# Optimization experiments

Measured on AMD Instinct MI355X. Metric: run time of the kernel, lower is better.

Reference implementation:

```python
import jax, jax.numpy as jnp
import numpy as np

B, L, C, H = 16, 680, 1024, 16
PATCH_NUMS = [1, 4, 9, 16, 25, 36, 64, 100, 169, 256]  # per-scale token counts, sum == L
MAX_SCALE_LOG = float(np.log(100.0))


def setup_inputs() -> dict:
    key = jax.random.key(0)
    ks = jax.random.split(key, 4)
    return {
        "x": jax.random.normal(ks[0], (B, L, C), jnp.float32),
        "patch_nums": jnp.asarray(PATCH_NUMS, jnp.int32),
        "mat_qkv_w": (jax.random.normal(ks[1], (3 * C, C), jnp.float32) * 0.02),
        "q_bias": jnp.zeros((C,), jnp.float32),
        "v_bias": jnp.zeros((C,), jnp.float32),
        "scale_log": jnp.full((1, H, 1, 1), np.log(4.0), jnp.float32),
        "proj_w": (jax.random.normal(ks[2], (C, C), jnp.float32) * 0.02),
        "proj_b": jnp.zeros((C,), jnp.float32),
    }


def _l2norm(t):
    # F.normalize(dim=-1): x / max(||x||_2, eps)
    n = jnp.sqrt(jnp.sum(t * t, axis=-1, keepdims=True))
    return t / jnp.maximum(n, 1e-12)


def reference(x, patch_nums, mat_qkv_w, q_bias, v_bias, scale_log, proj_w, proj_b):
    b, l, c = x.shape
    h = scale_log.shape[1]
    d = c // h
    # fused QKV linear with bias = cat(q_bias, zeros, v_bias)
    bias = jnp.concatenate([q_bias, jnp.zeros_like(q_bias), v_bias])
    qkv = (x @ mat_qkv_w.T + bias).reshape(b, l, 3, h, d)
    q, k, v = qkv[:, :, 0], qkv[:, :, 1], qkv[:, :, 2]  # [B, L, H, D]
    # attn_l2_norm path: scale=1, learned per-head multiplier on normalized q
    scale_mul = jnp.exp(jnp.minimum(scale_log, MAX_SCALE_LOG)).transpose(0, 2, 1, 3)  # (1,1,H,1)
    q = _l2norm(q) * scale_mul
    k = _l2norm(k)
    # training path: block-diagonal varlen attention, one block per scale
    pn = np.asarray(patch_nums).tolist()  # static scale schedule
    outs, start = [], 0
    for ln in pn:
        qs = q[:, start:start + ln]
        ks_ = k[:, start:start + ln]
        vs = v[:, start:start + ln]
        s = jnp.einsum("bihd,bjhd->bhij", qs, ks_)  # softmax_scale = 1
        a = jax.nn.softmax(s, axis=-1)
        outs.append(jnp.einsum("bhij,bjhd->bihd", a, vs))
        start += ln
    oup = jnp.concatenate(outs, axis=1).reshape(b, l, c)
    return oup @ proj_w.T + proj_b
```

## Files before the change

### kernel.cpp

```cpp
#include <hip/hip_runtime.h>

typedef __attribute__((ext_vector_type(8))) short bf16x8;
typedef __attribute__((ext_vector_type(4))) float f32x4;

#define Hh   16
#define Ll   680
#define Cc   1024
#define Bb   16
#define NSEG 10
#define LPAD 720

__device__ __forceinline__ unsigned short f32_bf16(float f) {
  union { float f; unsigned int u; } x; x.f = f;
  unsigned int r = x.u + 0x7FFFu + ((x.u >> 16) & 1u);
  return (unsigned short)(r >> 16);
}
__device__ __forceinline__ float bf16_f32(unsigned short u) {
  union { unsigned int u; float f; } x; x.u = ((unsigned int)u) << 16;
  return x.f;
}

__device__ __forceinline__ void async_copy16(const unsigned short* g, unsigned short* l) {
  __builtin_amdgcn_global_load_lds(
      (const __attribute__((address_space(1))) unsigned int*)g,
      (__attribute__((address_space(3))) unsigned int*)l, 16, 0, 0);
}

__device__ __constant__ int c_start2[11] = {0,1,5,14,30,55,91,155,255,424,680};
__device__ __constant__ int c_ps[NSEG]   = {0,8,16,32,48,80,120,184,288,464};
__device__ __constant__ int c_seg[16]    = {0,1,2,3,4,5,6,7,7,8,8,8,9,9,9,9};
__device__ __constant__ int c_tile0[16]  = {0,0,0,0,0,0,0,0,4,0,4,8,0,4,8,12};
__device__ __constant__ int c_len[NSEG]  = {1,4,9,16,25,36,64,100,169,256};

struct PlTab { unsigned short v[Ll]; };
constexpr PlTab make_pl() {
  PlTab t{};
  int starts[11] = {0,1,5,14,30,55,91,155,255,424,680};
  int ps[10]     = {0,8,16,32,48,80,120,184,288,464};
  for (int s = 0; s < 10; ++s)
    for (int l = starts[s]; l < starts[s + 1]; ++l)
      t.v[l] = (unsigned short)(l - starts[s] + ps[s]);
  return t;
}
__device__ __constant__ PlTab c_plt = make_pl();

__global__ __launch_bounds__(256) void conv_all(const float* __restrict__ x,
                                                const float* __restrict__ wqkv,
                                                const float* __restrict__ wproj,
                                                unsigned short* __restrict__ xb,
                                                unsigned short* __restrict__ wqkvb,
                                                unsigned short* __restrict__ wprojb) {
  const size_t n1 = (size_t)Bb * Ll * Cc;
  const size_t n2 = n1 + (size_t)3 * Cc * Cc;
  const size_t n3 = n2 + (size_t)Cc * Cc;
  size_t i = ((size_t)blockIdx.x * 256 + threadIdx.x) * 4;
  if (i >= n3) return;
  const float* src; unsigned short* dst; size_t off;
  if (i < n1)      { src = x;     dst = xb;     off = i; }
  else if (i < n2) { src = wqkv;  dst = wqkvb;  off = i - n1; }
  else             { src = wproj; dst = wprojb; off = i - n2; }
  float4 v = *reinterpret_cast<const float4*>(src + off);
  ushort4 o;
  o.x = f32_bf16(v.x); o.y = f32_bf16(v.y); o.z = f32_bf16(v.z); o.w = f32_bf16(v.w);
  *reinterpret_cast<ushort4*>(dst + off) = o;
}

__global__ __launch_bounds__(512, 2) void gemm_qkv(const unsigned short* __restrict__ A,
                                                   const unsigned short* __restrict__ Bm,
                                                   const float* __restrict__ qb,
                                                   const float* __restrict__ vb,
                                                   unsigned short* __restrict__ qn,
                                                   unsigned short* __restrict__ kn,
                                                   unsigned short* __restrict__ vtb) {
  __shared__ __align__(16) unsigned short lds[73728];
  const int t = threadIdx.x;
  const int lane = t & 63, w = t >> 6;
  const int col = lane & 15, quad = lane >> 4;
  const int wn = (w >> 1) * 64;
  const int m0 = blockIdx.y * 128, n0 = blockIdx.x * 256;
  const int bhs = wn >> 7;

  auto stageA = [&](int d3, int hs, int k0) {
    int kc = k0 > 960 ? 960 : k0;
    int r = t >> 3;
    int part = (t & 7) ^ (r & 7);
    async_copy16(A + (size_t)(m0 + hs * 64 + r) * 1024 + kc + part * 8,
                 lds + (d3 * 2 + hs) * 4096 + w * 512);
  };
  auto stageB = [&](int d3, int hs, int k0) {
    int kc = k0 > 960 ? 960 : k0;
#pragma unroll
    for (int i = 0; i < 2; ++i) {
      int c = i * 512 + t;
      int r = c >> 3;
      int part = (c & 7) ^ (r & 7);
      async_copy16(Bm + (size_t)(n0 + hs * 128 + r) * 1024 + kc + part * 8,
                   lds + 24576 + (d3 * 2 + hs) * 8192 + (i * 512 + w * 64) * 8);
    }
  };

  f32x4 acc[4][4];
#pragma unroll
  for (int i = 0; i < 4; ++i)
#pragma unroll
    for (int j = 0; j < 4; ++j)
#pragma unroll
      for (int r = 0; r < 4; ++r) acc[i][j][r] = 0.f;

#pragma unroll
  for (int tt = 0; tt < 2; ++tt) {
    stageB(tt, 0, tt * 64); stageA(tt, 0, tt * 64);
    stageB(tt, 1, tt * 64); stageA(tt, 1, tt * 64);
  }
  stageB(2, 0, 128); stageA(2, 0, 128);
  asm volatile("s_waitcnt vmcnt(9)" ::: "memory");
  __builtin_amdgcn_s_barrier();
  __builtin_amdgcn_sched_barrier(0);

  int bsel = 0;
  for (int tt = 0; tt < 16; ++tt) {
    const int b  = bsel;
    const int b2 = (bsel + 2 >= 3) ? bsel - 1 : bsel + 2;
    const unsigned short* As0 = lds + (b * 2 + 0) * 4096;
    const unsigned short* As1 = lds + (b * 2 + 1) * 4096;
    const unsigned short* Bs  = lds + 24576 + (b * 2 + bhs) * 8192;
    bf16x8 bfr[4][2], af[2][2];

#pragma unroll
    for (int nf = 0; nf < 4; ++nf) {
      int rb = (wn & 64) + nf * 16 + col;
#pragma unroll
      for (int kq = 0; kq < 2; ++kq)
        bfr[nf][kq] = *reinterpret_cast<const bf16x8*>(
            &Bs[(rb * 8 + ((kq * 4 + quad) ^ (col & 7))) * 8]);
    }
#pragma unroll
    for (int j = 0; j < 2; ++j) {
      int ri = (w & 1) * 32 + j * 16 + col;
#pragma unroll
      for (int kq = 0; kq < 2; ++kq)
        af[j][kq] = *reinterpret_cast<const bf16x8*>(
            &As0[(ri * 8 + ((kq * 4 + quad) ^ (col & 7))) * 8]);
    }
    stageB(b2, 1, (tt + 2) * 64);
    stageA(b2, 1, (tt + 2) * 64);
    __builtin_amdgcn_s_barrier();
    __builtin_amdgcn_s_setprio(1);
#pragma unroll
    for (int j = 0; j < 2; ++j)
#pragma unroll
      for (int nf = 0; nf < 4; ++nf)
#pragma unroll
        for (int kq = 0; kq < 2; ++kq)
          acc[j][nf] = __builtin_amdgcn_mfma_f32_16x16x32_bf16(af[j][kq], bfr[nf][kq],
                                                               acc[j][nf], 0, 0, 0);
    __builtin_amdgcn_s_setprio(0);
    __builtin_amdgcn_sched_barrier(0);
    asm volatile("s_waitcnt vmcnt(6)" ::: "memory");
    __builtin_amdgcn_s_barrier();
    __builtin_amdgcn_sched_barrier(0);

#pragma unroll
    for (int j = 0; j < 2; ++j) {
      int ri = (w & 1) * 32 + j * 16 + col;
#pragma unroll
      for (int kq = 0; kq < 2; ++kq)
        af[j][kq] = *reinterpret_cast<const bf16x8*>(
            &As1[(ri * 8 + ((kq * 4 + quad) ^ (col & 7))) * 8]);
    }
    stageB(b, 0, (tt + 3) * 64);
    stageA(b, 0, (tt + 3) * 64);
    __builtin_amdgcn_s_barrier();
    __builtin_amdgcn_s_setprio(1);
#pragma unroll
    for (int j = 0; j < 2; ++j)
#pragma unroll
      for (int nf = 0; nf < 4; ++nf)
#pragma unroll
        for (int kq = 0; kq < 2; ++kq)
          acc[2 + j][nf] = __builtin_amdgcn_mfma_f32_16x16x32_bf16(af[j][kq], bfr[nf][kq],
                                                                   acc[2 + j][nf], 0, 0, 0);
    __builtin_amdgcn_s_setprio(0);
    __builtin_amdgcn_sched_barrier(0);
    asm volatile("s_waitcnt vmcnt(9)" ::: "memory");
    __builtin_amdgcn_s_barrier();
    __builtin_amdgcn_sched_barrier(0);

    bsel = (bsel == 2) ? 0 : bsel + 1;
  }

  const int nbase = n0 + wn;
  const int field = nbase >> 10;
  const int h = (nbase >> 6) & 15;

  if (field < 2) {
    float scl[4][4];
    if (field == 1) {
#pragma unroll
      for (int mi = 0; mi < 4; ++mi)
#pragma unroll
        for (int r = 0; r < 4; ++r) {
          float s = 0.f;
#pragma unroll
          for (int ni = 0; ni < 4; ++ni) s += acc[mi][ni][r] * acc[mi][ni][r];
          s += __shfl_xor(s, 1); s += __shfl_xor(s, 2);
          s += __shfl_xor(s, 4); s += __shfl_xor(s, 8);
          scl[mi][r] = 1.f / fmaxf(sqrtf(s), 1e-12f);
        }
    }
    unsigned short* dst0 = (field == 0) ? qn : kn;
#pragma unroll
    for (int ni = 0; ni < 4; ++ni) {
      const int d = ni * 16 + col;
      const float bv = (field == 0) ? qb[h * 64 + d] : 0.f;
#pragma unroll
      for (int mi = 0; mi < 4; ++mi)
#pragma unroll
        for (int r = 0; r < 4; ++r) {
          int gm = m0 + (mi >> 1) * 64 + (w & 1) * 32 + (mi & 1) * 16 + quad * 4 + r;
          int b = gm / 680, l = gm - b * 680;
          float v = (field == 0) ? (acc[mi][ni][r] + bv) : (acc[mi][ni][r] * scl[mi][r]);
          dst0[((size_t)(b * Hh + h) * Ll + l) * 64 + d] = f32_bf16(v);
        }
    }
  } else {
#pragma unroll
    for (int mi = 0; mi < 4; ++mi) {
      int pl4[4], bb4[4];
#pragma unroll
      for (int r = 0; r < 4; ++r) {
        int gm = m0 + (mi >> 1) * 64 + (w & 1) * 32 + (mi & 1) * 16 + quad * 4 + r;
        int b = gm / 680, l = gm - b * 680;
        pl4[r] = c_plt.v[l];
        bb4[r] = b;
      }
#pragma unroll
      for (int ni = 0; ni < 4; ++ni) {
        const int d = ni * 16 + col;
        const float bv = vb[h * 64 + d];
#pragma unroll
        for (int r = 0; r < 4; ++r)
          vtb[((size_t)(bb4[r] * Hh + h) * 64 + d) * LPAD + pl4[r]] =
              f32_bf16(acc[mi][ni][r] + bv);
      }
    }
  }
}

__global__ __launch_bounds__(256) void gemm_bt(const unsigned short* __restrict__ A,
                                               const unsigned short* __restrict__ Bm,
                                               const float* __restrict__ bias,
                                               float* __restrict__ outp,
                                               int M, int N, int K) {
  __shared__ __align__(16) unsigned short As[128 * 64];
  __shared__ __align__(16) unsigned short Bs[128 * 64];
  const int t = threadIdx.x;
  const int lane = t & 63, w = t >> 6;
  const int col = lane & 15, quad = lane >> 4;
  const int wm = (w & 1) * 64, wn = (w >> 1) * 64;
  const int m0 = blockIdx.y * 128, n0 = blockIdx.x * 128;

  f32x4 acc[4][4];
#pragma unroll
  for (int i = 0; i < 4; ++i)
#pragma unroll
    for (int j = 0; j < 4; ++j)
#pragma unroll
      for (int r = 0; r < 4; ++r) acc[i][j][r] = 0.f;

  const int cbase = w * 256 + lane;
  for (int k0 = 0; k0 < K; k0 += 64) {
    __syncthreads();
#pragma unroll
    for (int i = 0; i < 4; ++i) {
      int c = cbase + i * 64;
      int r = c >> 3;
      int part = (c & 7) ^ (r & 7);
      async_copy16(A + (size_t)(m0 + r) * K + k0 + part * 8, As + (w * 256 + i * 64) * 8);
      async_copy16(Bm + (size_t)(n0 + r) * K + k0 + part * 8, Bs + (w * 256 + i * 64) * 8);
    }
    __syncthreads();
#pragma unroll
    for (int kk = 0; kk < 64; kk += 32) {
      const int p = (kk >> 3) + quad;
      bf16x8 af[4], bfr[4];
#pragma unroll
      for (int mi = 0; mi < 4; ++mi) {
        int row = wm + mi * 16 + col;
        af[mi] = *reinterpret_cast<const bf16x8*>(&As[(row * 8 + (p ^ (col & 7))) * 8]);
      }
#pragma unroll
      for (int ni = 0; ni < 4; ++ni) {
        int row = wn + ni * 16 + col;
        bfr[ni] = *reinterpret_cast<const bf16x8*>(&Bs[(row * 8 + (p ^ (col & 7))) * 8]);
      }
#pragma unroll
      for (int mi = 0; mi < 4; ++mi)
#pragma unroll
        for (int ni = 0; ni < 4; ++ni)
          acc[mi][ni] = __builtin_amdgcn_mfma_f32_16x16x32_bf16(af[mi], bfr[ni], acc[mi][ni], 0, 0, 0);
    }
  }
#pragma unroll
  for (int mi = 0; mi < 4; ++mi)
#pragma unroll
    for (int ni = 0; ni < 4; ++ni) {
      int gn = n0 + wn + ni * 16 + col;
      float bv = bias[gn];
#pragma unroll
      for (int r = 0; r < 4; ++r) {
        int gm = m0 + wm + mi * 16 + quad * 4 + r;
        outp[(size_t)gm * N + gn] = acc[mi][ni][r] + bv;
      }
    }
}

__global__ __launch_bounds__(256) void attn_kernel(const unsigned short* __restrict__ qn,
                                                   const unsigned short* __restrict__ kn,
                                                   const unsigned short* __restrict__ vtb,
                                                   const float* __restrict__ slog,
                                                   unsigned short* __restrict__ outb) {
  __shared__ __align__(16) unsigned short Ks[128 * 64];
  __shared__ __align__(16) unsigned short Vs[64 * 128];
  __shared__ __align__(16) unsigned short Ps[4 * 16 * 132];

  const int t = threadIdx.x;
  const int lane = t & 63, w = t >> 6;
  const int col = lane & 15, quad = lane >> 4;
  const int wi = blockIdx.x >> 8, bh = blockIdx.x & 255;
  const int h = bh & 15;
  const int seg = c_seg[wi];
  const int start = c_start2[seg], ln = c_len[seg], ps = c_ps[seg];
  const int njt = (ln + 15) >> 4;
  const int nchunk = (njt + 7) >> 3;
  const int qt = c_tile0[wi] + w;
  const bool qvalid = qt < njt;
  const float smul = __expf(fminf(slog[h], 4.6051701859880914f));

  const int qi = qt * 16 + col;
  const unsigned short* qrow = qn + ((size_t)bh * Ll + start + qi) * 64;
  bf16x8 qf0 = *reinterpret_cast<const bf16x8*>(qrow + quad * 8);
  bf16x8 qf1 = *reinterpret_cast<const bf16x8*>(qrow + 32 + quad * 8);
  {
    float ss = 0.f;
#pragma unroll
    for (int e = 0; e < 8; ++e) {
      float f0 = bf16_f32((unsigned short)qf0[e]), f1 = bf16_f32((unsigned short)qf1[e]);
      ss += f0 * f0 + f1 * f1;
    }
    ss += __shfl_xor(ss, 16);
    ss += __shfl_xor(ss, 32);
    const float qsc = smul / fmaxf(sqrtf(ss), 1e-12f);
#pragma unroll
    for (int e = 0; e < 8; ++e) {
      qf0[e] = (short)f32_bf16(bf16_f32((unsigned short)qf0[e]) * qsc);
      qf1[e] = (short)f32_bf16(bf16_f32((unsigned short)qf1[e]) * qsc);
    }
  }

  f32x4 o[4];
#pragma unroll
  for (int nt = 0; nt < 4; ++nt)
#pragma unroll
    for (int r = 0; r < 4; ++r) o[nt][r] = 0.f;
  float m4[4] = {-1e30f, -1e30f, -1e30f, -1e30f};
  float l4[4] = {0.f, 0.f, 0.f, 0.f};

  const int jc_t = (t & 15) ^ (t >> 4);

  for (int ch = 0; ch < nchunk; ++ch) {
    const int jbase = ch * 128;
    const int jtc = (njt - ch * 8 > 8) ? 8 : (njt - ch * 8);
    const int jtcp = (jtc + 1) & ~1;
    const int rowsK = jtc * 16;
    const int jcmax = jtcp * 2;
    __syncthreads();

#pragma unroll
    for (int i = 0; i < 4; ++i) {
      int c = i * 256 + w * 64 + lane;
      int jr = c >> 3;
      if (jr < rowsK) {
        int cc = (c & 7) ^ (jr & 7);
        async_copy16(kn + ((size_t)bh * Ll + start + jbase + jr) * 64 + cc * 8,
                     Ks + (i * 256 + w * 64) * 8);
      }
    }
    if (jc_t < jcmax) {
#pragma unroll
      for (int i = 0; i < 4; ++i) {
        int d = i * 16 + (t >> 4);
        async_copy16(vtb + ((size_t)bh * 64 + d) * LPAD + ps + jbase + jc_t * 8,
                     Vs + (i * 256 + w * 64) * 8);
      }
    }
    __syncthreads();

    f32x4 sf[8];
#pragma unroll
    for (int jt = 0; jt < 8; ++jt) {
      if (jt >= jtcp) continue;
      f32x4 s;
#pragma unroll
      for (int r = 0; r < 4; ++r) s[r] = 0.f;
      if (jt < jtc) {
        int jrow = jt * 16 + col;
        bf16x8 k0 = *reinterpret_cast<const bf16x8*>(&Ks[(jrow * 8 + (quad ^ (jrow & 7))) * 8]);
        bf16x8 k1 = *reinterpret_cast<const bf16x8*>(&Ks[(jrow * 8 + ((4 + quad) ^ (jrow & 7))) * 8]);
        s = __builtin_amdgcn_mfma_f32_16x16x32_bf16(qf0, k0, s, 0, 0, 0);
        s = __builtin_amdgcn_mfma_f32_16x16x32_bf16(qf1, k1, s, 0, 0, 0);
      }
      if (jbase + jt * 16 + col >= ln) {
#pragma unroll
        for (int r = 0; r < 4; ++r) s[r] = -1e30f;
      }
      sf[jt] = s;
    }
    float mc[4];
#pragma unroll
    for (int r = 0; r < 4; ++r) mc[r] = sf[0][r];
#pragma unroll
    for (int jt = 1; jt < 8; ++jt) {
      if (jt >= jtcp) continue;
#pragma unroll
      for (int r = 0; r < 4; ++r) mc[r] = fmaxf(mc[r], sf[jt][r]);
    }
#pragma unroll
    for (int mask = 1; mask <= 8; mask <<= 1)
#pragma unroll
      for (int r = 0; r < 4; ++r) mc[r] = fmaxf(mc[r], __shfl_xor(mc[r], mask));
    float alpha[4];
#pragma unroll
    for (int r = 0; r < 4; ++r) {
      float mn = fmaxf(m4[r], mc[r]);
      alpha[r] = __expf(m4[r] - mn);
      m4[r] = mn;
    }
    float ls[4] = {0.f, 0.f, 0.f, 0.f};
#pragma unroll
    for (int jt = 0; jt < 8; ++jt) {
      if (jt >= jtcp) continue;
#pragma unroll
      for (int r = 0; r < 4; ++r) {
        float pv = __expf(sf[jt][r] - m4[r]);
        ls[r] += pv;
        Ps[(w * 16 + quad * 4 + r) * 132 + jt * 16 + col] = f32_bf16(pv);
      }
    }
#pragma unroll
    for (int mask = 1; mask <= 8; mask <<= 1)
#pragma unroll
      for (int r = 0; r < 4; ++r) ls[r] += __shfl_xor(ls[r], mask);
#pragma unroll
    for (int r = 0; r < 4; ++r) l4[r] = l4[r] * alpha[r] + ls[r];
#pragma unroll
    for (int nt = 0; nt < 4; ++nt)
#pragma unroll
      for (int r = 0; r < 4; ++r) o[nt][r] *= alpha[r];

#pragma unroll
    for (int kk2 = 0; kk2 < 4; ++kk2) {
      if (kk2 >= (jtcp >> 1)) continue;
      bf16x8 pf = *reinterpret_cast<const bf16x8*>(&Ps[(w * 16 + col) * 132 + kk2 * 32 + quad * 8]);
#pragma unroll
      for (int nt = 0; nt < 4; ++nt) {
        int d = nt * 16 + col;
        int slot = (kk2 * 4 + quad) ^ (d & 15);
        bf16x8 vf = *reinterpret_cast<const bf16x8*>(&Vs[(d * 16 + slot) * 8]);
        o[nt] = __builtin_amdgcn_mfma_f32_16x16x32_bf16(pf, vf, o[nt], 0, 0, 0);
      }
    }
  }

  if (qvalid) {
    float inv[4];
#pragma unroll
    for (int r = 0; r < 4; ++r) inv[r] = 1.f / l4[r];
    const int b = bh >> 4;
#pragma unroll
    for (int nt = 0; nt < 4; ++nt)
#pragma unroll
      for (int r = 0; r < 4; ++r) {
        int ri = qt * 16 + quad * 4 + r;
        if (ri < ln) {
          size_t off = ((size_t)b * Ll + start + ri) * Cc + h * 64 + nt * 16 + col;
          outb[off] = f32_bf16(o[nt][r] * inv[r]);
        }
      }
  }
}

extern "C" void kernel_launch(void* const* d_in, const int* in_sizes, int n_in,
                              void* d_out, int out_size, void* d_ws, size_t ws_size,
                              hipStream_t stream) {
  const float* x     = (const float*)d_in[0];
  const float* wqkv  = (const float*)d_in[2];
  const float* qbias = (const float*)d_in[3];
  const float* vbias = (const float*)d_in[4];
  const float* slog  = (const float*)d_in[5];
  const float* wproj = (const float*)d_in[6];
  const float* pbias = (const float*)d_in[7];
  float* out = (float*)d_out;

  const size_t nX  = (size_t)Bb * Ll * Cc;
  const size_t nWq = (size_t)3 * Cc * Cc;
  const size_t nWp = (size_t)Cc * Cc;
  const size_t nVt = (size_t)Bb * Hh * 64 * LPAD;

  char* p = (char*)d_ws;
  unsigned short* xb     = (unsigned short*)p;  p += nX * 2;
  unsigned short* wqkvb  = (unsigned short*)p;  p += nWq * 2;
  unsigned short* wprojb = (unsigned short*)p;  p += nWp * 2;
  unsigned short* qn     = (unsigned short*)p;  p += nX * 2;
  unsigned short* kn     = (unsigned short*)p;  p += nX * 2;
  unsigned short* vtb    = (unsigned short*)p;  p += nVt * 2;
  unsigned short* attn   = xb;

  const size_t nAll = nX + nWq + nWp;
  conv_all<<<(int)(nAll / 1024), 256, 0, stream>>>(x, wqkv, wproj, xb, wqkvb, wprojb);

  gemm_qkv<<<dim3(12, 85), 512, 0, stream>>>(xb, wqkvb, qbias, vbias, qn, kn, vtb);
  attn_kernel<<<Bb * Hh * 16, 256, 0, stream>>>(qn, kn, vtb, slog, attn);
  gemm_bt<<<dim3(8, 85), 256, 0, stream>>>(attn, wprojb, pbias, out, 10880, 1024, 1024);
}
```

Before: 318.2 us.

## Rewrite projection GEMM with 128x256 tiles and triple-buffered async pipeline

The output projection GEMM moves from a single-buffered 128x128 tile with 256 threads to a 128x256 tile with 512 threads. K-slices are staged through a three-deep LDS ring using async global-to-LDS copies, with explicit vmcnt waits and barriers so loads overlap MFMA work, plus setprio around the MFMA bursts. This mirrors the pipelined QKV GEMM and targets load-latency stalls between the two syncthreads in the old loop. In exchange it uses about 144 KB of LDS per block and hardcodes the shapes, and the K-offset clamp at 960 issues redundant prefetch loads at the tail.

```diff
diff --git a/kernel.cpp b/kernel.cpp
--- a/kernel.cpp
+++ b/kernel.cpp
@@ -247,72 +247,139 @@
   }
 }
 
-__global__ __launch_bounds__(256) void gemm_bt(const unsigned short* __restrict__ A,
-                                               const unsigned short* __restrict__ Bm,
-                                               const float* __restrict__ bias,
-                                               float* __restrict__ outp,
-                                               int M, int N, int K) {
-  __shared__ __align__(16) unsigned short As[128 * 64];
-  __shared__ __align__(16) unsigned short Bs[128 * 64];
+__global__ __launch_bounds__(512, 2) void gemm_bt(const unsigned short* __restrict__ A,
+                                                  const unsigned short* __restrict__ Bm,
+                                                  const float* __restrict__ bias,
+                                                  float* __restrict__ outp) {
+  __shared__ __align__(16) unsigned short lds[73728];
   const int t = threadIdx.x;
   const int lane = t & 63, w = t >> 6;
   const int col = lane & 15, quad = lane >> 4;
-  const int wm = (w & 1) * 64, wn = (w >> 1) * 64;
-  const int m0 = blockIdx.y * 128, n0 = blockIdx.x * 128;
-
-  f32x4 acc[4][4];
-#pragma unroll
-  for (int i = 0; i < 4; ++i)
-#pragma unroll
-    for (int j = 0; j < 4; ++j)
-#pragma unroll
-      for (int r = 0; r < 4; ++r) acc[i][j][r] = 0.f;
-
-  const int cbase = w * 256 + lane;
-  for (int k0 = 0; k0 < K; k0 += 64) {
-    __syncthreads();
-#pragma unroll
-    for (int i = 0; i < 4; ++i) {
-      int c = cbase + i * 64;
+  const int wn = (w >> 1) * 64;
+  const int m0 = blockIdx.y * 128, n0 = blockIdx.x * 256;
+  const int bhs = wn >> 7;
+
+  auto stageA = [&](int d3, int hs, int k0) {
+    int kc = k0 > 960 ? 960 : k0;
+    int r = t >> 3;
+    int part = (t & 7) ^ (r & 7);
+    async_copy16(A + (size_t)(m0 + hs * 64 + r) * 1024 + kc + part * 8,
+                 lds + (d3 * 2 + hs) * 4096 + w * 512);
+  };
+  auto stageB = [&](int d3, int hs, int k0) {
+    int kc = k0 > 960 ? 960 : k0;
+#pragma unroll
+    for (int i = 0; i < 2; ++i) {
+      int c = i * 512 + t;
       int r = c >> 3;
       int part = (c & 7) ^ (r & 7);
-      async_copy16(A + (size_t)(m0 + r) * K + k0 + part * 8, As + (w * 256 + i * 64) * 8);
-      async_copy16(Bm + (size_t)(n0 + r) * K + k0 + part * 8, Bs + (w * 256 + i * 64) * 8);
-    }
-    __syncthreads();
-#pragma unroll
-    for (int kk = 0; kk < 64; kk += 32) {
-      const int p = (kk >> 3) + quad;
-      bf16x8 af[4], bfr[4];
-#pragma unroll
-      for (int mi = 0; mi < 4; ++mi) {
-        int row = wm + mi * 16 + col;
-        af[mi] = *reinterpret_cast<const bf16x8*>(&As[(row * 8 + (p ^ (col & 7))) * 8]);
-      }
-#pragma unroll
-      for (int ni = 0; ni < 4; ++ni) {
-        int row = wn + ni * 16 + col;
-        bfr[ni] = *reinterpret_cast<const bf16x8*>(&Bs[(row * 8 + (p ^ (col & 7))) * 8]);
-      }
-#pragma unroll
-      for (int mi = 0; mi < 4; ++mi)
-#pragma unroll
-        for (int ni = 0; ni < 4; ++ni)
-          acc[mi][ni] = __builtin_amdgcn_mfma_f32_16x16x32_bf16(af[mi], bfr[ni], acc[mi][ni], 0, 0, 0);
-    }
-  }
-#pragma unroll
-  for (int mi = 0; mi < 4; ++mi)
-#pragma unroll
-    for (int ni = 0; ni < 4; ++ni) {
-      int gn = n0 + wn + ni * 16 + col;
-      float bv = bias[gn];
+      async_copy16(Bm + (size_t)(n0 + hs * 128 + r) * 1024 + kc + part * 8,
+                   lds + 24576 + (d3 * 2 + hs) * 8192 + (i * 512 + w * 64) * 8);
+    }
+  };
+
+  f32x4 acc[4][4];
+#pragma unroll
+  for (int i = 0; i < 4; ++i)
+#pragma unroll
+    for (int j = 0; j < 4; ++j)
+#pragma unroll
+      for (int r = 0; r < 4; ++r) acc[i][j][r] = 0.f;
+
+#pragma unroll
+  for (int tt = 0; tt < 2; ++tt) {
+    stageB(tt, 0, tt * 64); stageA(tt, 0, tt * 64);
+    stageB(tt, 1, tt * 64); stageA(tt, 1, tt * 64);
+  }
+  stageB(2, 0, 128); stageA(2, 0, 128);
+  asm volatile("s_waitcnt vmcnt(9)" ::: "memory");
+  __builtin_amdgcn_s_barrier();
+  __builtin_amdgcn_sched_barrier(0);
+
+  int bsel = 0;
+  for (int tt = 0; tt < 16; ++tt) {
+    const int b  = bsel;
+    const int b2 = (bsel + 2 >= 3) ? bsel - 1 : bsel + 2;
+    const unsigned short* As0 = lds + (b * 2 + 0) * 4096;
+    const unsigned short* As1 = lds + (b * 2 + 1) * 4096;
+    const unsigned short* Bs  = lds + 24576 + (b * 2 + bhs) * 8192;
+    bf16x8 bfr[4][2], af[2][2];
+
+#pragma unroll
+    for (int nf = 0; nf < 4; ++nf) {
+      int rb = (wn & 64) + nf * 16 + col;
+#pragma unroll
+      for (int kq = 0; kq < 2; ++kq)
+        bfr[nf][kq] = *reinterpret_cast<const bf16x8*>(
+            &Bs[(rb * 8 + ((kq * 4 + quad) ^ (col & 7))) * 8]);
+    }
+#pragma unroll
+    for (int j = 0; j < 2; ++j) {
+      int ri = (w & 1) * 32 + j * 16 + col;
+#pragma unroll
+      for (int kq = 0; kq < 2; ++kq)
+        af[j][kq] = *reinterpret_cast<const bf16x8*>(
+            &As0[(ri * 8 + ((kq * 4 + quad) ^ (col & 7))) * 8]);
+    }
+    stageB(b2, 1, (tt + 2) * 64);
+    stageA(b2, 1, (tt + 2) * 64);
+    __builtin_amdgcn_s_barrier();
+    __builtin_amdgcn_s_setprio(1);
+#pragma unroll
+    for (int j = 0; j < 2; ++j)
+#pragma unroll
+      for (int nf = 0; nf < 4; ++nf)
+#pragma unroll
+        for (int kq = 0; kq < 2; ++kq)
+          acc[j][nf] = __builtin_amdgcn_mfma_f32_16x16x32_bf16(af[j][kq], bfr[nf][kq],
+                                                               acc[j][nf], 0, 0, 0);
+    __builtin_amdgcn_s_setprio(0);
+    __builtin_amdgcn_sched_barrier(0);
+    asm volatile("s_waitcnt vmcnt(6)" ::: "memory");
+    __builtin_amdgcn_s_barrier();
+    __builtin_amdgcn_sched_barrier(0);
+
+#pragma unroll
+    for (int j = 0; j < 2; ++j) {
+      int ri = (w & 1) * 32 + j * 16 + col;
+#pragma unroll
+      for (int kq = 0; kq < 2; ++kq)
+        af[j][kq] = *reinterpret_cast<const bf16x8*>(
+            &As1[(ri * 8 + ((kq * 4 + quad) ^ (col & 7))) * 8]);
+    }
+    stageB(b, 0, (tt + 3) * 64);
+    stageA(b, 0, (tt + 3) * 64);
+    __builtin_amdgcn_s_barrier();
+    __builtin_amdgcn_s_setprio(1);
+#pragma unroll
+    for (int j = 0; j < 2; ++j)
+#pragma unroll
+      for (int nf = 0; nf < 4; ++nf)
+#pragma unroll
+        for (int kq = 0; kq < 2; ++kq)
+          acc[2 + j][nf] = __builtin_amdgcn_mfma_f32_16x16x32_bf16(af[j][kq], bfr[nf][kq],
+                                                                   acc[2 + j][nf], 0, 0, 0);
+    __builtin_amdgcn_s_setprio(0);
+    __builtin_amdgcn_sched_barrier(0);
+    asm volatile("s_waitcnt vmcnt(9)" ::: "memory");
+    __builtin_amdgcn_s_barrier();
+    __builtin_amdgcn_sched_barrier(0);
+
+    bsel = (bsel == 2) ? 0 : bsel + 1;
+  }
+
+#pragma unroll
+  for (int ni = 0; ni < 4; ++ni) {
+    const int gn = n0 + wn + ni * 16 + col;
+    const float bv = bias[gn];
+#pragma unroll
+    for (int mi = 0; mi < 4; ++mi)
 #pragma unroll
       for (int r = 0; r < 4; ++r) {
-        int gm = m0 + wm + mi * 16 + quad * 4 + r;
-        outp[(size_t)gm * N + gn] = acc[mi][ni][r] + bv;
-      }
-    }
+        int gm = m0 + (mi >> 1) * 64 + (w & 1) * 32 + (mi & 1) * 16 + quad * 4 + r;
+        outp[(size_t)gm * 1024 + gn] = acc[mi][ni][r] + bv;
+      }
+  }
 }
 
 __global__ __launch_bounds__(256) void attn_kernel(const unsigned short* __restrict__ qn,
@@ -521,5 +588,5 @@
 
   gemm_qkv<<<dim3(12, 85), 512, 0, stream>>>(xb, wqkvb, qbias, vbias, qn, kn, vtb);
   attn_kernel<<<Bb * Hh * 16, 256, 0, stream>>>(qn, kn, vtb, slog, attn);
-  gemm_bt<<<dim3(8, 85), 256, 0, stream>>>(attn, wprojb, pbias, out, 10880, 1024, 1024);
-}
+  gemm_bt<<<dim3(4, 85), 512, 0, stream>>>(attn, wprojb, pbias, out);
+}
```

Result: slower. 338.7 us (+6.4%).

## Process all segments per (batch, head) in one 512-thread attention block

Applied to the files above, without the earlier changes.

The attention kernel now launches one 512-thread block per (batch, head) instead of 16 blocks per (batch, head). Each block loops serially over all ten scale segments, with every warp holding up to two query tiles, so the K/V tiles of a segment are loaded into shared memory once rather than by several blocks. The aim is to cut redundant K/V traffic and launch overhead. The cost is far fewer blocks, only about one per CU, and a serial chain of segments with block-wide barriers, which could reduce latency hiding and occupancy.

```diff
diff --git a/kernel.cpp b/kernel.cpp
--- a/kernel.cpp
+++ b/kernel.cpp
@@ -28,8 +28,6 @@
 
 __device__ __constant__ int c_start2[11] = {0,1,5,14,30,55,91,155,255,424,680};
 __device__ __constant__ int c_ps[NSEG]   = {0,8,16,32,48,80,120,184,288,464};
-__device__ __constant__ int c_seg[16]    = {0,1,2,3,4,5,6,7,7,8,8,8,9,9,9,9};
-__device__ __constant__ int c_tile0[16]  = {0,0,0,0,0,0,0,0,4,0,4,8,0,4,8,12};
 __device__ __constant__ int c_len[NSEG]  = {1,4,9,16,25,36,64,100,169,256};
 
 struct PlTab { unsigned short v[Ll]; };
@@ -315,178 +313,192 @@
     }
 }
 
-__global__ __launch_bounds__(256) void attn_kernel(const unsigned short* __restrict__ qn,
-                                                   const unsigned short* __restrict__ kn,
-                                                   const unsigned short* __restrict__ vtb,
-                                                   const float* __restrict__ slog,
-                                                   unsigned short* __restrict__ outb) {
+__global__ __launch_bounds__(512, 2) void attn_kernel(const unsigned short* __restrict__ qn,
+                                                      const unsigned short* __restrict__ kn,
+                                                      const unsigned short* __restrict__ vtb,
+                                                      const float* __restrict__ slog,
+                                                      unsigned short* __restrict__ outb) {
   __shared__ __align__(16) unsigned short Ks[128 * 64];
   __shared__ __align__(16) unsigned short Vs[64 * 128];
-  __shared__ __align__(16) unsigned short Ps[4 * 16 * 132];
+  __shared__ __align__(16) unsigned short Ps[8 * 16 * 132];
 
   const int t = threadIdx.x;
   const int lane = t & 63, w = t >> 6;
   const int col = lane & 15, quad = lane >> 4;
-  const int wi = blockIdx.x >> 8, bh = blockIdx.x & 255;
+  const int bh = blockIdx.x;
   const int h = bh & 15;
-  const int seg = c_seg[wi];
-  const int start = c_start2[seg], ln = c_len[seg], ps = c_ps[seg];
-  const int njt = (ln + 15) >> 4;
-  const int nchunk = (njt + 7) >> 3;
-  const int qt = c_tile0[wi] + w;
-  const bool qvalid = qt < njt;
+  const int bb = bh >> 4;
   const float smul = __expf(fminf(slog[h], 4.6051701859880914f));
 
-  const int qi = qt * 16 + col;
-  const unsigned short* qrow = qn + ((size_t)bh * Ll + start + qi) * 64;
-  bf16x8 qf0 = *reinterpret_cast<const bf16x8*>(qrow + quad * 8);
-  bf16x8 qf1 = *reinterpret_cast<const bf16x8*>(qrow + 32 + quad * 8);
-  {
-    float ss = 0.f;
-#pragma unroll
-    for (int e = 0; e < 8; ++e) {
-      float f0 = bf16_f32((unsigned short)qf0[e]), f1 = bf16_f32((unsigned short)qf1[e]);
-      ss += f0 * f0 + f1 * f1;
-    }
-    ss += __shfl_xor(ss, 16);
-    ss += __shfl_xor(ss, 32);
-    const float qsc = smul / fmaxf(sqrtf(ss), 1e-12f);
-#pragma unroll
-    for (int e = 0; e < 8; ++e) {
-      qf0[e] = (short)f32_bf16(bf16_f32((unsigned short)qf0[e]) * qsc);
-      qf1[e] = (short)f32_bf16(bf16_f32((unsigned short)qf1[e]) * qsc);
-    }
-  }
-
-  f32x4 o[4];
-#pragma unroll
-  for (int nt = 0; nt < 4; ++nt)
-#pragma unroll
-    for (int r = 0; r < 4; ++r) o[nt][r] = 0.f;
-  float m4[4] = {-1e30f, -1e30f, -1e30f, -1e30f};
-  float l4[4] = {0.f, 0.f, 0.f, 0.f};
-
-  const int jc_t = (t & 15) ^ (t >> 4);
-
-  for (int ch = 0; ch < nchunk; ++ch) {
-    const int jbase = ch * 128;
-    const int jtc = (njt - ch * 8 > 8) ? 8 : (njt - ch * 8);
-    const int jtcp = (jtc + 1) & ~1;
-    const int rowsK = jtc * 16;
-    const int jcmax = jtcp * 2;
-    __syncthreads();
-
-#pragma unroll
-    for (int i = 0; i < 4; ++i) {
-      int c = i * 256 + w * 64 + lane;
-      int jr = c >> 3;
-      if (jr < rowsK) {
-        int cc = (c & 7) ^ (jr & 7);
-        async_copy16(kn + ((size_t)bh * Ll + start + jbase + jr) * 64 + cc * 8,
-                     Ks + (i * 256 + w * 64) * 8);
-      }
-    }
-    if (jc_t < jcmax) {
-#pragma unroll
-      for (int i = 0; i < 4; ++i) {
-        int d = i * 16 + (t >> 4);
-        async_copy16(vtb + ((size_t)bh * 64 + d) * LPAD + ps + jbase + jc_t * 8,
-                     Vs + (i * 256 + w * 64) * 8);
-      }
-    }
-    __syncthreads();
-
-    f32x4 sf[8];
-#pragma unroll
-    for (int jt = 0; jt < 8; ++jt) {
-      if (jt >= jtcp) continue;
-      f32x4 s;
-#pragma unroll
-      for (int r = 0; r < 4; ++r) s[r] = 0.f;
-      if (jt < jtc) {
-        int jrow = jt * 16 + col;
-        bf16x8 k0 = *reinterpret_cast<const bf16x8*>(&Ks[(jrow * 8 + (quad ^ (jrow & 7))) * 8]);
-        bf16x8 k1 = *reinterpret_cast<const bf16x8*>(&Ks[(jrow * 8 + ((4 + quad) ^ (jrow & 7))) * 8]);
-        s = __builtin_amdgcn_mfma_f32_16x16x32_bf16(qf0, k0, s, 0, 0, 0);
-        s = __builtin_amdgcn_mfma_f32_16x16x32_bf16(qf1, k1, s, 0, 0, 0);
-      }
-      if (jbase + jt * 16 + col >= ln) {
-#pragma unroll
-        for (int r = 0; r < 4; ++r) s[r] = -1e30f;
-      }
-      sf[jt] = s;
-    }
-    float mc[4];
-#pragma unroll
-    for (int r = 0; r < 4; ++r) mc[r] = sf[0][r];
-#pragma unroll
-    for (int jt = 1; jt < 8; ++jt) {
-      if (jt >= jtcp) continue;
-#pragma unroll
-      for (int r = 0; r < 4; ++r) mc[r] = fmaxf(mc[r], sf[jt][r]);
-    }
-#pragma unroll
-    for (int mask = 1; mask <= 8; mask <<= 1)
-#pragma unroll
-      for (int r = 0; r < 4; ++r) mc[r] = fmaxf(mc[r], __shfl_xor(mc[r], mask));
-    float alpha[4];
-#pragma unroll
-    for (int r = 0; r < 4; ++r) {
-      float mn = fmaxf(m4[r], mc[r]);
-      alpha[r] = __expf(m4[r] - mn);
-      m4[r] = mn;
-    }
-    float ls[4] = {0.f, 0.f, 0.f, 0.f};
-#pragma unroll
-    for (int jt = 0; jt < 8; ++jt) {
-      if (jt >= jtcp) continue;
-#pragma unroll
-      for (int r = 0; r < 4; ++r) {
-        float pv = __expf(sf[jt][r] - m4[r]);
-        ls[r] += pv;
-        Ps[(w * 16 + quad * 4 + r) * 132 + jt * 16 + col] = f32_bf16(pv);
-      }
-    }
-#pragma unroll
-    for (int mask = 1; mask <= 8; mask <<= 1)
-#pragma unroll
-      for (int r = 0; r < 4; ++r) ls[r] += __shfl_xor(ls[r], mask);
-#pragma unroll
-    for (int r = 0; r < 4; ++r) l4[r] = l4[r] * alpha[r] + ls[r];
-#pragma unroll
-    for (int nt = 0; nt < 4; ++nt)
-#pragma unroll
-      for (int r = 0; r < 4; ++r) o[nt][r] *= alpha[r];
-
-#pragma unroll
-    for (int kk2 = 0; kk2 < 4; ++kk2) {
-      if (kk2 >= (jtcp >> 1)) continue;
-      bf16x8 pf = *reinterpret_cast<const bf16x8*>(&Ps[(w * 16 + col) * 132 + kk2 * 32 + quad * 8]);
-#pragma unroll
-      for (int nt = 0; nt < 4; ++nt) {
-        int d = nt * 16 + col;
-        int slot = (kk2 * 4 + quad) ^ (d & 15);
-        bf16x8 vf = *reinterpret_cast<const bf16x8*>(&Vs[(d * 16 + slot) * 8]);
-        o[nt] = __builtin_amdgcn_mfma_f32_16x16x32_bf16(pf, vf, o[nt], 0, 0, 0);
-      }
-    }
-  }
-
-  if (qvalid) {
-    float inv[4];
-#pragma unroll
-    for (int r = 0; r < 4; ++r) inv[r] = 1.f / l4[r];
-    const int b = bh >> 4;
-#pragma unroll
-    for (int nt = 0; nt < 4; ++nt)
-#pragma unroll
-      for (int r = 0; r < 4; ++r) {
-        int ri = qt * 16 + quad * 4 + r;
-        if (ri < ln) {
-          size_t off = ((size_t)b * Ll + start + ri) * Cc + h * 64 + nt * 16 + col;
-          outb[off] = f32_bf16(o[nt][r] * inv[r]);
-        }
-      }
+  for (int seg = 0; seg < NSEG; ++seg) {
+    const int start = c_start2[seg], ln = c_len[seg], ps = c_ps[seg];
+    const int njt = (ln + 15) >> 4;
+    const int nchunk = (njt + 7) >> 3;
+
+    bf16x8 qf0[2], qf1[2];
+#pragma unroll
+    for (int s = 0; s < 2; ++s) {
+      const int qt = w + s * 8;
+      const int qi = qt * 16 + col;
+      const unsigned short* qrow = qn + ((size_t)bh * Ll + start + qi) * 64;
+      qf0[s] = *reinterpret_cast<const bf16x8*>(qrow + quad * 8);
+      qf1[s] = *reinterpret_cast<const bf16x8*>(qrow + 32 + quad * 8);
+      float ss = 0.f;
+#pragma unroll
+      for (int e = 0; e < 8; ++e) {
+        float f0 = bf16_f32((unsigned short)qf0[s][e]), f1 = bf16_f32((unsigned short)qf1[s][e]);
+        ss += f0 * f0 + f1 * f1;
+      }
+      ss += __shfl_xor(ss, 16);
+      ss += __shfl_xor(ss, 32);
+      const float qsc = smul / fmaxf(sqrtf(ss), 1e-12f);
+#pragma unroll
+      for (int e = 0; e < 8; ++e) {
+        qf0[s][e] = (short)f32_bf16(bf16_f32((unsigned short)qf0[s][e]) * qsc);
+        qf1[s][e] = (short)f32_bf16(bf16_f32((unsigned short)qf1[s][e]) * qsc);
+      }
+    }
+
+    f32x4 o[2][4];
+    float m4[2][4], l4[2][4];
+#pragma unroll
+    for (int s = 0; s < 2; ++s) {
+#pragma unroll
+      for (int nt = 0; nt < 4; ++nt)
+#pragma unroll
+        for (int r = 0; r < 4; ++r) o[s][nt][r] = 0.f;
+#pragma unroll
+      for (int r = 0; r < 4; ++r) { m4[s][r] = -1e30f; l4[s][r] = 0.f; }
+    }
+
+    for (int ch = 0; ch < nchunk; ++ch) {
+      const int jbase = ch * 128;
+      const int jtc = (njt - ch * 8 > 8) ? 8 : (njt - ch * 8);
+      const int jtcp = (jtc + 1) & ~1;
+      const int rowsK = jtc * 16;
+      const int jcmax = jtcp * 2;
+      __syncthreads();
+
+#pragma unroll
+      for (int i = 0; i < 2; ++i) {
+        int c = i * 512 + t;
+        int jr = c >> 3;
+        if (jr < rowsK) {
+          int cc = (c & 7) ^ (jr & 7);
+          async_copy16(kn + ((size_t)bh * Ll + start + jbase + jr) * 64 + cc * 8,
+                       Ks + (i * 512 + w * 64) * 8);
+        }
+      }
+#pragma unroll
+      for (int i = 0; i < 2; ++i) {
+        int d = i * 32 + (t >> 4);
+        int jc = (t & 15) ^ ((t >> 4) & 15);
+        if (jc < jcmax)
+          async_copy16(vtb + ((size_t)bh * 64 + d) * LPAD + ps + jbase + jc * 8,
+                       Vs + (i * 512 + w * 64) * 8);
+      }
+      __syncthreads();
+
+#pragma unroll
+      for (int s = 0; s < 2; ++s) {
+        const int qt = w + s * 8;
+        if (qt >= njt) continue;
+
+        f32x4 sf[8];
+#pragma unroll
+        for (int jt = 0; jt < 8; ++jt) {
+          if (jt >= jtcp) continue;
+          f32x4 sv;
+#pragma unroll
+          for (int r = 0; r < 4; ++r) sv[r] = 0.f;
+          if (jt < jtc) {
+            int jrow = jt * 16 + col;
+            bf16x8 k0 = *reinterpret_cast<const bf16x8*>(&Ks[(jrow * 8 + (quad ^ (jrow & 7))) * 8]);
+            bf16x8 k1 = *reinterpret_cast<const bf16x8*>(&Ks[(jrow * 8 + ((4 + quad) ^ (jrow & 7))) * 8]);
+            sv = __builtin_amdgcn_mfma_f32_16x16x32_bf16(qf0[s], k0, sv, 0, 0, 0);
+            sv = __builtin_amdgcn_mfma_f32_16x16x32_bf16(qf1[s], k1, sv, 0, 0, 0);
+          }
+          if (jbase + jt * 16 + col >= ln) {
+#pragma unroll
+            for (int r = 0; r < 4; ++r) sv[r] = -1e30f;
+          }
+          sf[jt] = sv;
+        }
+        float mc[4];
+#pragma unroll
+        for (int r = 0; r < 4; ++r) mc[r] = sf[0][r];
+#pragma unroll
+        for (int jt = 1; jt < 8; ++jt) {
+          if (jt >= jtcp) continue;
+#pragma unroll
+          for (int r = 0; r < 4; ++r) mc[r] = fmaxf(mc[r], sf[jt][r]);
+        }
+#pragma unroll
+        for (int mask = 1; mask <= 8; mask <<= 1)
+#pragma unroll
+          for (int r = 0; r < 4; ++r) mc[r] = fmaxf(mc[r], __shfl_xor(mc[r], mask));
+        float alpha[4];
+#pragma unroll
+        for (int r = 0; r < 4; ++r) {
+          float mn = fmaxf(m4[s][r], mc[r]);
+          alpha[r] = __expf(m4[s][r] - mn);
+          m4[s][r] = mn;
+        }
+        float lsum[4] = {0.f, 0.f, 0.f, 0.f};
+#pragma unroll
+        for (int jt = 0; jt < 8; ++jt) {
+          if (jt >= jtcp) continue;
+#pragma unroll
+          for (int r = 0; r < 4; ++r) {
+            float pv = __expf(sf[jt][r] - m4[s][r]);
+            lsum[r] += pv;
+            Ps[(w * 16 + quad * 4 + r) * 132 + jt * 16 + col] = f32_bf16(pv);
+          }
+        }
+#pragma unroll
+        for (int mask = 1; mask <= 8; mask <<= 1)
+#pragma unroll
+          for (int r = 0; r < 4; ++r) lsum[r] += __shfl_xor(lsum[r], mask);
+#pragma unroll
+        for (int r = 0; r < 4; ++r) l4[s][r] = l4[s][r] * alpha[r] + lsum[r];
+#pragma unroll
+        for (int nt = 0; nt < 4; ++nt)
+#pragma unroll
+          for (int r = 0; r < 4; ++r) o[s][nt][r] *= alpha[r];
+
+#pragma unroll
+        for (int kk2 = 0; kk2 < 4; ++kk2) {
+          if (kk2 >= (jtcp >> 1)) continue;
+          bf16x8 pf = *reinterpret_cast<const bf16x8*>(&Ps[(w * 16 + col) * 132 + kk2 * 32 + quad * 8]);
+#pragma unroll
+          for (int nt = 0; nt < 4; ++nt) {
+            int d = nt * 16 + col;
+            int slot = (kk2 * 4 + quad) ^ (d & 15);
+            bf16x8 vf = *reinterpret_cast<const bf16x8*>(&Vs[(d * 16 + slot) * 8]);
+            o[s][nt] = __builtin_amdgcn_mfma_f32_16x16x32_bf16(pf, vf, o[s][nt], 0, 0, 0);
+          }
+        }
+      }
+    }
+
+#pragma unroll
+    for (int s = 0; s < 2; ++s) {
+      const int qt = w + s * 8;
+      if (qt >= njt) continue;
+      float inv[4];
+#pragma unroll
+      for (int r = 0; r < 4; ++r) inv[r] = 1.f / l4[s][r];
+#pragma unroll
+      for (int nt = 0; nt < 4; ++nt)
+#pragma unroll
+        for (int r = 0; r < 4; ++r) {
+          int ri = qt * 16 + quad * 4 + r;
+          if (ri < ln) {
+            size_t off = ((size_t)bb * Ll + start + ri) * Cc + h * 64 + nt * 16 + col;
+            outb[off] = f32_bf16(o[s][nt][r] * inv[r]);
+          }
+        }
+    }
   }
 }
 
@@ -520,6 +532,6 @@
   conv_all<<<(int)(nAll / 1024), 256, 0, stream>>>(x, wqkv, wproj, xb, wqkvb, wprojb);
 
   gemm_qkv<<<dim3(12, 85), 512, 0, stream>>>(xb, wqkvb, qbias, vbias, qn, kn, vtb);
-  attn_kernel<<<Bb * Hh * 16, 256, 0, stream>>>(qn, kn, vtb, slog, attn);
+  attn_kernel<<<Bb * Hh, 512, 0, stream>>>(qn, kn, vtb, slog, attn);
   gemm_bt<<<dim3(8, 85), 256, 0, stream>>>(attn, wprojb, pbias, out, 10880, 1024, 1024);
 }
```

New measurement: 325.9 us. 1.02x slower.
